# Kernel optimization log

Hardware: AMD Instinct MI355X
Metric: run time of the kernel (lower is better)

Reference implementation:

```python
import jax, jax.numpy as jnp
from jax import lax
import numpy as np

K = 32        # self.k: neighbors queried per center
TOP = 5       # inner topk size (hardcoded in source)
MAX_ITER = 16 # bound on the data-dependent while loop; leftovers emitted at final iter


def _refine_one(pc, centers, ids):
    """Vectorized translation of the per-batch while-loop.

    Instead of shrinking the sample set each iteration (data-dependent shape),
    every sample is tracked with an `active` flag and a convergence-iteration
    stamp. Emitting order in the torch code is (iteration, surviving-order),
    and boolean masking preserves relative original order, so a stable sort by
    (conv_iter, original_index) reproduces the exact concatenation order.
    """
    N, D = pc.shape
    S = centers.shape[0]
    ar = jnp.arange(S)

    def knn(q):  # q: [S,3] -> [S,K] indices of nearest cloud points (ascending dist)
        d2 = jnp.sum((q[:, None, :] - pc[None, :, :]) ** 2, axis=-1)  # [S,N]
        _, ind = lax.top_k(-d2, K)
        return ind

    def step(cur_pts, cur_idx):
        ind = knn(cur_pts)                                   # [S,K]
        nbh = pc[ind]                                        # [S,K,3]
        gc = jnp.mean(nbh, axis=1)                           # [S,3]
        dist = jnp.linalg.norm(nbh - gc[:, None, :], axis=2) # [S,K]
        _, top = lax.top_k(-dist, TOP)                       # [S,TOP] smallest dists
        in_top = jnp.any(top == 0, axis=1)                   # center (col 0) stable?
        new_idx = ind[ar, top[:, 0]]                         # point closest to centroid
        return ind, in_top, new_idx

    def body(it, st):
        cur_pts, cur_idx, conv_it, out_pts, out_idx, out_grp, active = st
        ind, in_top, new_idx = step(cur_pts, cur_idx)
        newly = active & in_top
        conv_it = jnp.where(newly, it, conv_it)
        out_pts = jnp.where(newly[:, None], cur_pts, out_pts)
        out_idx = jnp.where(newly, cur_idx, out_idx)
        out_grp = jnp.where(newly[:, None], ind, out_grp)
        move = active & ~in_top
        cur_idx = jnp.where(move, new_idx, cur_idx)
        cur_pts = jnp.where(move[:, None], pc[new_idx], cur_pts)
        return (cur_pts, cur_idx, conv_it, out_pts, out_idx, out_grp, move)

    st0 = (centers, ids,
           jnp.full((S,), MAX_ITER, jnp.int32),
           jnp.zeros((S, D), pc.dtype),
           jnp.zeros((S,), ids.dtype),
           jnp.zeros((S, K), jnp.int32),
           jnp.ones((S,), bool))
    cur_pts, cur_idx, conv_it, out_pts, out_idx, out_grp, active = lax.fori_loop(
        0, MAX_ITER, body, st0)

    # force-emit any sample that never converged within MAX_ITER
    ind, _, _ = step(cur_pts, cur_idx)
    out_pts = jnp.where(active[:, None], cur_pts, out_pts)
    out_idx = jnp.where(active, cur_idx, out_idx)
    out_grp = jnp.where(active[:, None], ind, out_grp)

    order = jnp.argsort(conv_it * (S + 1) + ar)  # stable (iter, orig-pos) order
    return out_pts[order], out_idx[order], out_grp[order]


def setup_inputs() -> dict:
    key = jax.random.key(0)
    k1, k2, k3 = jax.random.split(key, 3)
    B, N, S = 8, 8192, 1024
    xyz = jax.random.normal(k1, (B, N, 3), jnp.float32)
    center = jax.random.normal(k2, (B, S, 3), jnp.float32)
    idx = jax.random.randint(k3, (B, S), 0, N, jnp.int32)
    return {"xyz": xyz, "center": center, "idx": idx}


def reference(xyz, center, idx):
    assert xyz.shape[0] == center.shape[0]
    C, I1, I2 = jax.vmap(_refine_one)(xyz, center, idx)
    # torch runs under no_grad; outputs are detached constants
    return (lax.stop_gradient(C), I1, I2)
```

## Files before the change

kernel.cpp:

```cpp
#include <hip/hip_runtime.h>
#include <stdint.h>

#define BATCH   8
#define NPTS    8192
#define SCH     1024
#define KNN     32
#define TOPC    5
#define MAXIT   16
#define NCELL   4096
#define NGRP    128
#define NSEED   6

typedef unsigned long long ull;
typedef uint16_t u16;
typedef float vf2 __attribute__((ext_vector_type(2)));
typedef float vf4 __attribute__((ext_vector_type(4)));

#define SENTKEY ((((ull)0x7F800000u) << 13) | 0x1FFFull)

__device__ __forceinline__ float d2_exact(vf4 q, vf4 p) {
#pragma clang fp contract(off)
    vf2 d = q.xy - p.xy;
    vf2 s = d * d;
    float dz = q.z - p.z;
    float sz = dz * dz;
    return (s.x + s.y) + sz;
}

__device__ __forceinline__ void insert_top4(ull key, ull& k0, ull& k1, ull& k2,
                                            ull& k3, float& th) {
    if (key < k3) {
        k3 = key;
        { bool c = k3 < k2; ull mn = c ? k3 : k2, mx = c ? k2 : k3; k2 = mn; k3 = mx; }
        { bool c = k2 < k1; ull mn = c ? k2 : k1, mx = c ? k1 : k2; k1 = mn; k2 = mx; }
        { bool c = k1 < k0; ull mn = c ? k1 : k0, mx = c ? k0 : k1; k0 = mn; k1 = mx; }
        th = __uint_as_float((uint32_t)(k3 >> 13));
    }
}

__device__ __forceinline__ ull wave_min_u64(ull k) {
#pragma unroll
    for (int off = 32; off; off >>= 1) {
        ull o = (ull)__shfl_xor((unsigned long long)k, off, 64);
        k = o < k ? o : k;
    }
    return k;
}
__device__ __forceinline__ ull wave_max_u64(ull k) {
#pragma unroll
    for (int off = 32; off; off >>= 1) {
        ull o = (ull)__shfl_xor((unsigned long long)k, off, 64);
        k = o > k ? o : k;
    }
    return k;
}

__device__ __forceinline__ float bbox_mind2(vf4 q, vf4 c, vf4 h) {
    float dx = fmaxf(fabsf(q.x - c.x) - h.x, 0.f);
    float dy = fmaxf(fabsf(q.y - c.y) - h.y, 0.f);
    float dz = fmaxf(fabsf(q.z - c.z) - h.z, 0.f);
    return (dx * dx + dy * dy + dz * dz) * 0.9999f;
}

__device__ __forceinline__ ull cx(ull v, int xl, bool keepmin) {
    ull o = (ull)__shfl_xor((unsigned long long)v, xl, 64);
    return ((v < o) == keepmin) ? v : o;
}
__device__ __forceinline__ void cswap(ull& a, ull& b, bool up) {
    bool lt = a < b;
    ull mn = lt ? a : b, mx = lt ? b : a;
    a = up ? mn : mx;
    b = up ? mx : mn;
}

__device__ __forceinline__ void sort128(ull& s0, ull& s1, int lane) {
    cswap(s0, s1, true);
    if (lane & 1) { ull t = s0; s0 = s1; s1 = t; }
#pragma unroll
    for (int kk = 4; kk <= 128; kk <<= 1) {
        const bool up = (lane & (kk >> 1)) == 0;
#pragma unroll
        for (int d = kk >> 1; d >= 2; d >>= 1) {
            const int xl = d >> 1;
            const bool keepmin = (up == ((lane & xl) == 0));
            s0 = cx(s0, xl, keepmin);
            s1 = cx(s1, xl, keepmin);
        }
        cswap(s0, s1, up);
    }
}

__device__ __forceinline__ int next_gid(ull& r0, ull& r1) {
    if (r0) { int g = __ffsll((unsigned long long)r0) - 1; r0 &= r0 - 1; return g; }
    if (r1) { int g = __ffsll((unsigned long long)r1) - 1; r1 &= r1 - 1; return 64 + g; }
    return -1;
}

__device__ __forceinline__ int cell_of(float x, float y, float z) {
    int cxi = min(15, max(0, (int)floorf((x + 4.0f) * 2.0f)));
    int cyi = min(15, max(0, (int)floorf((y + 4.0f) * 2.0f)));
    int czi = min(15, max(0, (int)floorf((z + 4.0f) * 2.0f)));
    uint32_t sx = (cxi & 1) | ((cxi & 2) << 2) | ((cxi & 4) << 4) | ((cxi & 8) << 6);
    uint32_t sy = (cyi & 1) | ((cyi & 2) << 2) | ((cyi & 4) << 4) | ((cyi & 8) << 6);
    uint32_t sz = (czi & 1) | ((czi & 2) << 2) | ((czi & 4) << 4) | ((czi & 8) << 6);
    return (int)(sx | (sy << 1) | (sz << 2));
}

__device__ __attribute__((noinline)) int serial_topk_masked(
    const vf4* __restrict__ Psort, vf4 q, int lane, ull sm0, ull sm1) {
    ull k0 = SENTKEY, k1 = SENTKEY, k2 = SENTKEY, k3 = SENTKEY;
    int s0 = 0, s1 = 0, s2 = 0, s3 = 0;
    float th = __builtin_inff();
    for (int gid = 0; gid < NGRP; ++gid) {
        bool sel = (gid < 64) ? ((sm0 >> gid) & 1ull) : ((sm1 >> (gid - 64)) & 1ull);
        if (!sel) continue;
        vf4 p = Psort[(gid << 6) + lane];
        float d2 = d2_exact(q, p);
        uint32_t oi = __float_as_uint(p.w);
        ull key = ((ull)__float_as_uint(d2) << 13) | oi;
        if (d2 <= th && key < k3) {
            k3 = key; s3 = gid;
            if (k3 < k2) { ull t = k2; k2 = k3; k3 = t; int ts = s2; s2 = s3; s3 = ts; }
            if (k2 < k1) { ull t = k1; k1 = k2; k2 = t; int ts = s1; s1 = s2; s2 = ts; }
            if (k1 < k0) { ull t = k0; k0 = k1; k1 = t; int ts = s0; s0 = s1; s1 = ts; }
            th = __uint_as_float((uint32_t)(k3 >> 13));
        }
    }
    ull em0 = 0ull, em1 = 0ull;
    int cnt = 4, my_ind = 0;
    for (int r = 0; r < KNN; ++r) {
        ull gmin = wave_min_u64(k0);
        int widx = (int)(gmin & 0x1FFFull);
        if (lane == r) my_ind = widx;
        if (k0 == gmin) {
            int g = s0;
            if (g < 64) em0 |= 1ull << g; else em1 |= 1ull << (g - 64);
            k0 = k1; k1 = k2; k2 = k3; k3 = SENTKEY;
            s0 = s1; s1 = s2; s2 = s3;
            if (--cnt == 0) {
                k0 = k1 = k2 = k3 = SENTKEY;
                float th2 = __builtin_inff();
                for (int gid = 0; gid < NGRP; ++gid) {
                    bool sel = (gid < 64) ? ((sm0 >> gid) & 1ull)
                                          : ((sm1 >> (gid - 64)) & 1ull);
                    bool ex = (gid < 64) ? ((em0 >> gid) & 1ull)
                                         : ((em1 >> (gid - 64)) & 1ull);
                    if (!sel || ex) continue;
                    vf4 p = Psort[(gid << 6) + lane];
                    float d2 = d2_exact(q, p);
                    uint32_t oi = __float_as_uint(p.w);
                    ull key = ((ull)__float_as_uint(d2) << 13) | oi;
                    if (d2 <= th2 && key < k3) {
                        k3 = key; s3 = gid;
                        if (k3 < k2) { ull t = k2; k2 = k3; k3 = t; int ts = s2; s2 = s3; s3 = ts; }
                        if (k2 < k1) { ull t = k1; k1 = k2; k2 = t; int ts = s1; s1 = s2; s2 = ts; }
                        if (k1 < k0) { ull t = k0; k0 = k1; k1 = t; int ts = s0; s0 = s1; s1 = ts; }
                        th2 = __uint_as_float((uint32_t)(k3 >> 13));
                    }
                }
                cnt = 4;
            }
        }
    }
    return my_ind;
}

__global__ __launch_bounds__(256) void prep_kernel(const float* __restrict__ xyz,
                                                   vf4* __restrict__ pc4,
                                                   int* __restrict__ counts) {
    int i = (int)(blockIdx.x * blockDim.x + threadIdx.x);
    if (i >= BATCH * NPTS) return;
    vf4 v;
    v.x = xyz[(size_t)i * 3 + 0];
    v.y = xyz[(size_t)i * 3 + 1];
    v.z = xyz[(size_t)i * 3 + 2];
    v.w = 0.f;
    pc4[i] = v;
    int b = i >> 13;
    atomicAdd(&counts[b * NCELL + cell_of(v.x, v.y, v.z)], 1);
}

__global__ __launch_bounds__(1024) void scan_kernel(const int* __restrict__ counts,
                                                    int* __restrict__ cursor) {
    int b = (int)blockIdx.x, tid = (int)threadIdx.x;
    __shared__ int part[1024];
    int base = b * NCELL + tid * 4;
    int v0 = counts[base], v1 = counts[base + 1], v2 = counts[base + 2], v3 = counts[base + 3];
    int s = v0 + v1 + v2 + v3;
    part[tid] = s;
    __syncthreads();
    for (int off = 1; off < 1024; off <<= 1) {
        int t = (tid >= off) ? part[tid - off] : 0;
        __syncthreads();
        part[tid] += t;
        __syncthreads();
    }
    int excl = part[tid] - s;
    cursor[base] = excl;
    cursor[base + 1] = excl + v0;
    cursor[base + 2] = excl + v0 + v1;
    cursor[base + 3] = excl + v0 + v1 + v2;
}

__global__ __launch_bounds__(256) void scatter_kernel(const vf4* __restrict__ pc4,
                                                      int* __restrict__ cursor,
                                                      vf4* __restrict__ sortedP) {
    int i = (int)(blockIdx.x * blockDim.x + threadIdx.x);
    if (i >= BATCH * NPTS) return;
    vf4 v = pc4[i];
    int b = i >> 13, pi = i & (NPTS - 1);
    int c = cell_of(v.x, v.y, v.z);
    int pos = atomicAdd(&cursor[b * NCELL + c], 1);
    v.w = __uint_as_float((uint32_t)pi);
    sortedP[((size_t)b << 13) + pos] = v;
}

__global__ __launch_bounds__(256) void bbox_kernel(const vf4* __restrict__ sortedP,
                                                   vf4* __restrict__ bC,
                                                   vf4* __restrict__ bH) {
    int g = (int)((blockIdx.x * blockDim.x + threadIdx.x) >> 6);
    int lane = (int)(threadIdx.x & 63);
    vf4 p = sortedP[((size_t)g << 6) + lane];
    float mnx = p.x, mxx = p.x, mny = p.y, mxy = p.y, mnz = p.z, mxz = p.z;
#pragma unroll
    for (int off = 32; off; off >>= 1) {
        mnx = fminf(mnx, __shfl_xor(mnx, off, 64));
        mxx = fmaxf(mxx, __shfl_xor(mxx, off, 64));
        mny = fminf(mny, __shfl_xor(mny, off, 64));
        mxy = fmaxf(mxy, __shfl_xor(mxy, off, 64));
        mnz = fminf(mnz, __shfl_xor(mnz, off, 64));
        mxz = fmaxf(mxz, __shfl_xor(mxz, off, 64));
    }
    if (lane == 0) {
        vf4 c, h;
        c.x = (mnx + mxx) * 0.5f; c.y = (mny + mxy) * 0.5f; c.z = (mnz + mxz) * 0.5f; c.w = 0.f;
        h.x = (mxx - mnx) * 0.5f; h.y = (mxy - mny) * 0.5f; h.z = (mxz - mnz) * 0.5f; h.w = 0.f;
        bC[g] = c;
        bH[g] = h;
    }
}

__global__ __launch_bounds__(256) void refine_kernel(
    const vf4* __restrict__ pc4, const vf4* __restrict__ sortedP,
    const vf4* __restrict__ bC, const vf4* __restrict__ bH,
    const float* __restrict__ center, const int* __restrict__ idx_in,
    float* __restrict__ pts_ws, int* __restrict__ idx_ws,
    int* __restrict__ grp_ws, int* __restrict__ conv_ws) {
    const int lane = (int)(threadIdx.x & 63);
    const int w = (int)(threadIdx.x >> 6);
    const int wv = (int)((blockIdx.x * blockDim.x + threadIdx.x) >> 6);
    const int b = (int)(blockIdx.x >> 8);
    const vf4* __restrict__ Porig = pc4 + ((size_t)b << 13);
    const vf4* __restrict__ Psort = sortedP + ((size_t)b << 13);

    __shared__ vf4 sbC[NGRP], sbH[NGRP];
    __shared__ vf4 nbh[4][KNN];

    {
        const int t = (int)threadIdx.x;
        if (t < NGRP) sbC[t] = bC[(b << 7) + t];
        else          sbH[t - NGRP] = bH[(b << 7) + (t - NGRP)];
    }
    __syncthreads();

    const size_t ch = (size_t)wv;
    vf4 q;
    q.x = center[ch * 3 + 0];
    q.y = center[ch * 3 + 1];
    q.z = center[ch * 3 + 2];
    q.w = 0.f;
    int qidx = idx_in[ch];

    int conv = MAXIT;
    int my_ind = 0;
    vf4 myp = q;
    bool warm = false;

    for (int it = 0;; ++it) {
        const vf4 c0 = sbC[lane],      h0 = sbH[lane];
        const vf4 c1 = sbC[64 + lane], h1 = sbH[64 + lane];
        const float m0 = bbox_mind2(q, c0, h0);
        const float m1 = bbox_mind2(q, c1, h1);

        ull k0 = SENTKEY, k1 = SENTKEY, k2 = SENTKEY, k3 = SENTKEY;
        float th = __builtin_inff();
        ull sm0 = 0ull, sm1 = 0ull, am0 = 0ull, am1 = 0ull;
        float th0 = __builtin_inff();

        bool fastwarm = false;
        if (warm) {
            const float dw = (lane < KNN) ? d2_exact(q, myp) : 0.f;
            th0 = dw;
#pragma unroll
            for (int off = 32; off; off >>= 1)
                th0 = fmaxf(th0, __shfl_xor(th0, off, 64));
            sm0 = __ballot(m0 <= th0);
            sm1 = __ballot(m1 <= th0);
            const int nsel = __popcll(sm0) + __popcll(sm1);
            if (nsel <= 20) { fastwarm = true; am0 = sm0; am1 = sm1; }
        }

        if (!fastwarm) {
            sm0 = 0ull; sm1 = 0ull;
            ull g0k = ((ull)__float_as_uint(m0) << 7) | (uint32_t)lane;
            ull g1k = ((ull)__float_as_uint(m1) << 7) | (uint32_t)(64 + lane);
            sort128(g0k, g1k, lane);
#pragma unroll
            for (int r = 0; r < NSEED; ++r) {
                const ull nk = (r & 1)
                    ? (ull)__shfl((unsigned long long)g1k, r >> 1, 64)
                    : (ull)__shfl((unsigned long long)g0k, r >> 1, 64);
                const int gid = (int)(nk & 127ull);
                if (gid < 64) sm0 |= 1ull << gid; else sm1 |= 1ull << (gid - 64);
                const vf4 p = Psort[(gid << 6) + lane];
                const float d2 = d2_exact(q, p);
                if (d2 <= th)
                    insert_top4(((ull)__float_as_uint(d2) << 13) | __float_as_uint(p.w),
                                k0, k1, k2, k3, th);
            }
            ull t = k0;
            {
                ull o = (ull)__shfl_xor((unsigned long long)t, 32, 64);
                t = o < t ? o : t;
            }
            const ull B = wave_max_u64(t);
            const float Bd = fminf(__uint_as_float((uint32_t)(B >> 13)), th0);
            am0 = __ballot(m0 <= Bd) & ~sm0;
            am1 = __ballot(m1 <= Bd) & ~sm1;
            sm0 |= am0; sm1 |= am1;
        }

        {
            ull rem0 = am0, rem1 = am1;
            int ga = next_gid(rem0, rem1);
            while (ga >= 0) {
                const int gb = next_gid(rem0, rem1);
                const vf4 pa = Psort[(ga << 6) + lane];
                vf4 pb;
                if (gb >= 0) pb = Psort[(gb << 6) + lane];
                const float da = d2_exact(q, pa);
                if (da <= th)
                    insert_top4(((ull)__float_as_uint(da) << 13) | __float_as_uint(pa.w),
                                k0, k1, k2, k3, th);
                if (gb >= 0) {
                    const float dbv = d2_exact(q, pb);
                    if (dbv <= th)
                        insert_top4(((ull)__float_as_uint(dbv) << 13) | __float_as_uint(pb.w),
                                    k0, k1, k2, k3, th);
                }
                ga = next_gid(rem0, rem1);
            }
        }
        const ull prek3 = k3;

        const bool odd = (lane & 1) != 0;
        ull a0 = odd ? k3 : k0;
        ull a1 = odd ? k2 : k1;
        ull a2 = odd ? k1 : k2;
        ull a3 = odd ? k0 : k3;
#pragma unroll
        for (int kk = 8; kk <= 256; kk <<= 1) {
            const bool up = (lane & (kk >> 2)) == 0;
#pragma unroll
            for (int d = kk >> 1; d >= 4; d >>= 1) {
                const int xl = d >> 2;
                const bool keepmin = (up == ((lane & xl) == 0));
                a0 = cx(a0, xl, keepmin);
                a1 = cx(a1, xl, keepmin);
                a2 = cx(a2, xl, keepmin);
                a3 = cx(a3, xl, keepmin);
            }
            cswap(a0, a2, up); cswap(a1, a3, up);
            cswap(a0, a1, up); cswap(a2, a3, up);
        }
        const ull tau = (ull)__shfl((unsigned long long)a3, 7, 64);
        const ull bad = __ballot(prek3 < tau);
        if (bad != 0ull) {
            my_ind = serial_topk_masked(Psort, q, lane, sm0, sm1);
        } else {
            const int src = lane >> 2;
            const uint32_t lo0 = (uint32_t)__shfl((int)(uint32_t)a0, src, 64);
            const uint32_t lo1 = (uint32_t)__shfl((int)(uint32_t)a1, src, 64);
            const uint32_t lo2 = (uint32_t)__shfl((int)(uint32_t)a2, src, 64);
            const uint32_t lo3 = (uint32_t)__shfl((int)(uint32_t)a3, src, 64);
            const int sel = lane & 3;
            uint32_t lo = (sel == 0) ? lo0 : (sel == 1) ? lo1 : (sel == 2) ? lo2 : lo3;
            my_ind = (int)(lo & 0x1FFFu);
        }

        if (it == MAXIT) break;

        myp = q;
        if (lane < KNN) {
            myp = Porig[my_ind];
            nbh[w][lane] = myp;
        }
        __asm__ volatile("s_waitcnt lgkmcnt(0)" ::: "memory");
        float sx = 0.f, sy = 0.f, sz = 0.f;
#pragma unroll
        for (int j = 0; j < KNN; ++j) {
            vf4 pj = nbh[w][j];
            sx = __fadd_rn(sx, pj.x);
            sy = __fadd_rn(sy, pj.y);
            sz = __fadd_rn(sz, pj.z);
        }
        const float gx = __fmul_rn(sx, 0.03125f);
        const float gy = __fmul_rn(sy, 0.03125f);
        const float gz = __fmul_rn(sz, 0.03125f);

        float dj = __builtin_inff();
        if (lane < KNN) {
            const float dx = __fsub_rn(myp.x, gx);
            const float dy = __fsub_rn(myp.y, gy);
            const float dz = __fsub_rn(myp.z, gz);
            dj = sqrtf(__fadd_rn(__fadd_rn(__fmul_rn(dx, dx), __fmul_rn(dy, dy)),
                                 __fmul_rn(dz, dz)));
        }
        const uint32_t db = __float_as_uint(dj);
        const uint32_t d0 = (uint32_t)__shfl((int)db, 0, 64);
        const ull bal = __ballot(db < d0);
        if (__popcll(bal) <= TOPC - 1) { conv = it; break; }

        uint32_t m = db;
#pragma unroll
        for (int off = 32; off; off >>= 1) {
            uint32_t o = (uint32_t)__shfl_xor((int)m, off, 64);
            m = o < m ? o : m;
        }
        const ull balm = __ballot(db == m);
        const int jm = __ffsll((unsigned long long)balm) - 1;
        qidx = __shfl(my_ind, jm, 64);
        q.x = __shfl(myp.x, jm, 64);
        q.y = __shfl(myp.y, jm, 64);
        q.z = __shfl(myp.z, jm, 64);
        q.w = 0.f;
        warm = true;
    }

    if (lane < KNN) grp_ws[ch * KNN + lane] = my_ind;
    if (lane == 0) {
        pts_ws[ch * 3 + 0] = q.x;
        pts_ws[ch * 3 + 1] = q.y;
        pts_ws[ch * 3 + 2] = q.z;
        idx_ws[ch] = qidx;
        conv_ws[ch] = conv;
    }
}

__global__ __launch_bounds__(1024) void order_kernel(
    const float* __restrict__ pts_ws, const int* __restrict__ idx_ws,
    const int* __restrict__ grp_ws, const int* __restrict__ conv_ws,
    float* __restrict__ out) {
    const int b = (int)blockIdx.x;
    const int s = (int)threadIdx.x;
    const int w = s >> 6, l = s & 63;
    __shared__ int wavecnt[16][MAXIT + 1];
    __shared__ int binbase[MAXIT + 1];
    const size_t ch = (size_t)b * SCH + s;
    const int c = conv_ws[ch];
    int rw = 0;
#pragma unroll
    for (int v = 0; v <= MAXIT; ++v) {
        ull bal = __ballot(c == v);
        if (l == 0) wavecnt[w][v] = (int)__popcll(bal);
        if (c == v) rw = (int)__popcll(bal & ((1ull << l) - 1ull));
    }
    __syncthreads();
    if (s == 0) {
        int acc = 0;
        for (int v = 0; v <= MAXIT; ++v) {
            int t = 0;
            for (int w2 = 0; w2 < 16; ++w2) t += wavecnt[w2][v];
            binbase[v] = acc;
            acc += t;
        }
    }
    __syncthreads();
    int pos = binbase[c] + rw;
    for (int w2 = 0; w2 < w; ++w2) pos += wavecnt[w2][c];

    float* __restrict__ C  = out;
    float* __restrict__ I1 = out + (size_t)BATCH * SCH * 3;
    float* __restrict__ I2 = I1 + (size_t)BATCH * SCH;
    const size_t o = (size_t)b * SCH + pos;
    C[o * 3 + 0] = pts_ws[ch * 3 + 0];
    C[o * 3 + 1] = pts_ws[ch * 3 + 1];
    C[o * 3 + 2] = pts_ws[ch * 3 + 2];
    I1[o] = (float)idx_ws[ch];
#pragma unroll
    for (int k = 0; k < KNN; ++k) I2[o * KNN + k] = (float)grp_ws[ch * KNN + k];
}

extern "C" void kernel_launch(void* const* d_in, const int* in_sizes, int n_in,
                              void* d_out, int out_size, void* d_ws, size_t ws_size,
                              hipStream_t stream) {
    const float* xyz    = (const float*)d_in[0];
    const float* center = (const float*)d_in[1];
    const int*   idx_in = (const int*)d_in[2];
    float* out = (float*)d_out;

    char* wp = (char*)d_ws;
    vf4* pc4     = (vf4*)wp;  wp += (size_t)BATCH * NPTS * sizeof(vf4);
    vf4* sortedP = (vf4*)wp;  wp += (size_t)BATCH * NPTS * sizeof(vf4);
    vf4* bC      = (vf4*)wp;  wp += (size_t)BATCH * NGRP * sizeof(vf4);
    vf4* bH      = (vf4*)wp;  wp += (size_t)BATCH * NGRP * sizeof(vf4);
    int* counts  = (int*)wp;  wp += (size_t)BATCH * NCELL * 4;
    int* cursor  = (int*)wp;  wp += (size_t)BATCH * NCELL * 4;
    float* pts_ws = (float*)wp; wp += (size_t)BATCH * SCH * 3 * 4;
    int*   idx_ws = (int*)wp;   wp += (size_t)BATCH * SCH * 4;
    int*   grp_ws = (int*)wp;   wp += (size_t)BATCH * SCH * KNN * 4;
    int*   conv_ws = (int*)wp;

    hipMemsetAsync(counts, 0, (size_t)BATCH * NCELL * 4, stream);
    prep_kernel<<<(BATCH * NPTS + 255) / 256, 256, 0, stream>>>(xyz, pc4, counts);
    scan_kernel<<<BATCH, 1024, 0, stream>>>(counts, cursor);
    scatter_kernel<<<(BATCH * NPTS + 255) / 256, 256, 0, stream>>>(pc4, cursor, sortedP);
    bbox_kernel<<<(BATCH * NGRP * 64) / 256, 256, 0, stream>>>(sortedP, bC, bH);

    const int chains = BATCH * SCH;
    refine_kernel<<<chains * 64 / 256, 256, 0, stream>>>(
        pc4, sortedP, bC, bH, center, idx_in, pts_ws, idx_ws, grp_ws, conv_ws);
    order_kernel<<<BATCH, SCH, 0, stream>>>(pts_ws, idx_ws, grp_ws, conv_ws, out);
}
```

Measured before the change: 203.1 us.

## Fuse grid build into one per-batch kernel, sort 32-bit keys, tune launch bounds

Replaces the memset, prep, scan, scatter and bbox kernels with a single per-batch 1024-thread kernel. It builds the cell histogram in shared memory, does a wave-shuffle scan, scatters the points and computes the group bounding boxes, which removes several launches and global atomics. The group-distance bitonic sort now uses 32-bit keys made from truncated float bits instead of 64-bit keys, halving the shuffle traffic. Truncating the float bits may change the seed order when distances nearly tie, which could affect exactness. Launch bounds on refine_kernel are set to request 5 blocks per CU.

```diff
diff --git a/kernel.cpp b/kernel.cpp
--- a/kernel.cpp
+++ b/kernel.cpp
@@ -12,7 +12,6 @@
 #define NSEED   6
 
 typedef unsigned long long ull;
-typedef uint16_t u16;
 typedef float vf2 __attribute__((ext_vector_type(2)));
 typedef float vf4 __attribute__((ext_vector_type(4)));
 
@@ -73,9 +72,19 @@
     b = up ? mx : mn;
 }
 
-__device__ __forceinline__ void sort128(ull& s0, ull& s1, int lane) {
-    cswap(s0, s1, true);
-    if (lane & 1) { ull t = s0; s0 = s1; s1 = t; }
+__device__ __forceinline__ uint32_t cx32(uint32_t v, int xl, bool keepmin) {
+    uint32_t o = (uint32_t)__shfl_xor((int)v, xl, 64);
+    return ((v < o) == keepmin) ? v : o;
+}
+__device__ __forceinline__ void cswap32(uint32_t& a, uint32_t& b, bool up) {
+    uint32_t mn = a < b ? a : b, mx = a < b ? b : a;
+    a = up ? mn : mx;
+    b = up ? mx : mn;
+}
+
+__device__ __forceinline__ void sort128_u32(uint32_t& s0, uint32_t& s1, int lane) {
+    cswap32(s0, s1, true);
+    if (lane & 1) { uint32_t t = s0; s0 = s1; s1 = t; }
 #pragma unroll
     for (int kk = 4; kk <= 128; kk <<= 1) {
         const bool up = (lane & (kk >> 1)) == 0;
@@ -83,10 +92,10 @@
         for (int d = kk >> 1; d >= 2; d >>= 1) {
             const int xl = d >> 1;
             const bool keepmin = (up == ((lane & xl) == 0));
-            s0 = cx(s0, xl, keepmin);
-            s1 = cx(s1, xl, keepmin);
-        }
-        cswap(s0, s1, up);
+            s0 = cx32(s0, xl, keepmin);
+            s1 = cx32(s1, xl, keepmin);
+        }
+        cswap32(s0, s1, up);
     }
 }
 
@@ -165,82 +174,96 @@
     return my_ind;
 }
 
-__global__ __launch_bounds__(256) void prep_kernel(const float* __restrict__ xyz,
-                                                   vf4* __restrict__ pc4,
-                                                   int* __restrict__ counts) {
-    int i = (int)(blockIdx.x * blockDim.x + threadIdx.x);
-    if (i >= BATCH * NPTS) return;
-    vf4 v;
-    v.x = xyz[(size_t)i * 3 + 0];
-    v.y = xyz[(size_t)i * 3 + 1];
-    v.z = xyz[(size_t)i * 3 + 2];
-    v.w = 0.f;
-    pc4[i] = v;
-    int b = i >> 13;
-    atomicAdd(&counts[b * NCELL + cell_of(v.x, v.y, v.z)], 1);
-}
-
-__global__ __launch_bounds__(1024) void scan_kernel(const int* __restrict__ counts,
-                                                    int* __restrict__ cursor) {
-    int b = (int)blockIdx.x, tid = (int)threadIdx.x;
-    __shared__ int part[1024];
-    int base = b * NCELL + tid * 4;
-    int v0 = counts[base], v1 = counts[base + 1], v2 = counts[base + 2], v3 = counts[base + 3];
-    int s = v0 + v1 + v2 + v3;
-    part[tid] = s;
-    __syncthreads();
-    for (int off = 1; off < 1024; off <<= 1) {
-        int t = (tid >= off) ? part[tid - off] : 0;
-        __syncthreads();
-        part[tid] += t;
-        __syncthreads();
-    }
-    int excl = part[tid] - s;
-    cursor[base] = excl;
-    cursor[base + 1] = excl + v0;
-    cursor[base + 2] = excl + v0 + v1;
-    cursor[base + 3] = excl + v0 + v1 + v2;
-}
-
-__global__ __launch_bounds__(256) void scatter_kernel(const vf4* __restrict__ pc4,
-                                                      int* __restrict__ cursor,
-                                                      vf4* __restrict__ sortedP) {
-    int i = (int)(blockIdx.x * blockDim.x + threadIdx.x);
-    if (i >= BATCH * NPTS) return;
-    vf4 v = pc4[i];
-    int b = i >> 13, pi = i & (NPTS - 1);
-    int c = cell_of(v.x, v.y, v.z);
-    int pos = atomicAdd(&cursor[b * NCELL + c], 1);
-    v.w = __uint_as_float((uint32_t)pi);
-    sortedP[((size_t)b << 13) + pos] = v;
-}
-
-__global__ __launch_bounds__(256) void bbox_kernel(const vf4* __restrict__ sortedP,
-                                                   vf4* __restrict__ bC,
-                                                   vf4* __restrict__ bH) {
-    int g = (int)((blockIdx.x * blockDim.x + threadIdx.x) >> 6);
-    int lane = (int)(threadIdx.x & 63);
-    vf4 p = sortedP[((size_t)g << 6) + lane];
-    float mnx = p.x, mxx = p.x, mny = p.y, mxy = p.y, mnz = p.z, mxz = p.z;
-#pragma unroll
-    for (int off = 32; off; off >>= 1) {
-        mnx = fminf(mnx, __shfl_xor(mnx, off, 64));
-        mxx = fmaxf(mxx, __shfl_xor(mxx, off, 64));
-        mny = fminf(mny, __shfl_xor(mny, off, 64));
-        mxy = fmaxf(mxy, __shfl_xor(mxy, off, 64));
-        mnz = fminf(mnz, __shfl_xor(mnz, off, 64));
-        mxz = fmaxf(mxz, __shfl_xor(mxz, off, 64));
-    }
-    if (lane == 0) {
-        vf4 c, h;
-        c.x = (mnx + mxx) * 0.5f; c.y = (mny + mxy) * 0.5f; c.z = (mnz + mxz) * 0.5f; c.w = 0.f;
-        h.x = (mxx - mnx) * 0.5f; h.y = (mxy - mny) * 0.5f; h.z = (mxz - mnz) * 0.5f; h.w = 0.f;
-        bC[g] = c;
-        bH[g] = h;
-    }
-}
-
-__global__ __launch_bounds__(256) void refine_kernel(
+__global__ __launch_bounds__(1024) void build_kernel(const float* __restrict__ xyz,
+                                                     vf4* __restrict__ pc4,
+                                                     vf4* __restrict__ sortedP,
+                                                     vf4* __restrict__ bC,
+                                                     vf4* __restrict__ bH) {
+    const int b = (int)blockIdx.x;
+    const int t = (int)threadIdx.x;
+    const int lane = t & 63, w = t >> 6;
+    __shared__ int hist[NCELL];
+    __shared__ int wsum[16];
+
+    for (int i = t; i < NCELL; i += 1024) hist[i] = 0;
+    __syncthreads();
+
+    const float* __restrict__ X = xyz + (size_t)b * NPTS * 3;
+    vf4 pt[8];
+    int pcell[8];
+#pragma unroll
+    for (int k = 0; k < 8; ++k) {
+        const int i = k * 1024 + t;
+        vf4 v;
+        v.x = X[i * 3 + 0];
+        v.y = X[i * 3 + 1];
+        v.z = X[i * 3 + 2];
+        v.w = 0.f;
+        pt[k] = v;
+        pc4[(size_t)b * NPTS + i] = v;
+        const int c = cell_of(v.x, v.y, v.z);
+        pcell[k] = c;
+        atomicAdd(&hist[c], 1);
+    }
+    __syncthreads();
+
+    const int base = t * 4;
+    const int v0 = hist[base], v1 = hist[base + 1], v2 = hist[base + 2], v3 = hist[base + 3];
+    const int s = v0 + v1 + v2 + v3;
+    int incl = s;
+#pragma unroll
+    for (int off = 1; off < 64; off <<= 1) {
+        int o = __shfl_up(incl, off, 64);
+        if (lane >= off) incl += o;
+    }
+    if (lane == 63) wsum[w] = incl;
+    __syncthreads();
+    if (t == 0) {
+        int acc = 0;
+#pragma unroll
+        for (int i = 0; i < 16; ++i) { int x = wsum[i]; wsum[i] = acc; acc += x; }
+    }
+    __syncthreads();
+    const int excl = incl - s + wsum[w];
+    hist[base]     = excl;
+    hist[base + 1] = excl + v0;
+    hist[base + 2] = excl + v0 + v1;
+    hist[base + 3] = excl + v0 + v1 + v2;
+    __syncthreads();
+
+#pragma unroll
+    for (int k = 0; k < 8; ++k) {
+        const int i = k * 1024 + t;
+        const int pos = atomicAdd(&hist[pcell[k]], 1);
+        vf4 v = pt[k];
+        v.w = __uint_as_float((uint32_t)i);
+        sortedP[((size_t)b << 13) + pos] = v;
+    }
+    __syncthreads();
+
+    for (int g = w; g < NGRP; g += 16) {
+        vf4 p = sortedP[((size_t)b << 13) + (g << 6) + lane];
+        float mnx = p.x, mxx = p.x, mny = p.y, mxy = p.y, mnz = p.z, mxz = p.z;
+#pragma unroll
+        for (int off = 32; off; off >>= 1) {
+            mnx = fminf(mnx, __shfl_xor(mnx, off, 64));
+            mxx = fmaxf(mxx, __shfl_xor(mxx, off, 64));
+            mny = fminf(mny, __shfl_xor(mny, off, 64));
+            mxy = fmaxf(mxy, __shfl_xor(mxy, off, 64));
+            mnz = fminf(mnz, __shfl_xor(mnz, off, 64));
+            mxz = fmaxf(mxz, __shfl_xor(mxz, off, 64));
+        }
+        if (lane == 0) {
+            vf4 c, h;
+            c.x = (mnx + mxx) * 0.5f; c.y = (mny + mxy) * 0.5f; c.z = (mnz + mxz) * 0.5f; c.w = 0.f;
+            h.x = (mxx - mnx) * 0.5f; h.y = (mxy - mny) * 0.5f; h.z = (mxz - mnz) * 0.5f; h.w = 0.f;
+            bC[(b << 7) + g] = c;
+            bH[(b << 7) + g] = h;
+        }
+    }
+}
+
+__global__ __launch_bounds__(256, 5) void refine_kernel(
     const vf4* __restrict__ pc4, const vf4* __restrict__ sortedP,
     const vf4* __restrict__ bC, const vf4* __restrict__ bH,
     const float* __restrict__ center, const int* __restrict__ idx_in,
@@ -302,15 +325,15 @@
 
         if (!fastwarm) {
             sm0 = 0ull; sm1 = 0ull;
-            ull g0k = ((ull)__float_as_uint(m0) << 7) | (uint32_t)lane;
-            ull g1k = ((ull)__float_as_uint(m1) << 7) | (uint32_t)(64 + lane);
-            sort128(g0k, g1k, lane);
+            uint32_t g0k = ((__float_as_uint(m0) >> 6) << 7) | (uint32_t)lane;
+            uint32_t g1k = ((__float_as_uint(m1) >> 6) << 7) | (uint32_t)(64 + lane);
+            sort128_u32(g0k, g1k, lane);
 #pragma unroll
             for (int r = 0; r < NSEED; ++r) {
-                const ull nk = (r & 1)
-                    ? (ull)__shfl((unsigned long long)g1k, r >> 1, 64)
-                    : (ull)__shfl((unsigned long long)g0k, r >> 1, 64);
-                const int gid = (int)(nk & 127ull);
+                const uint32_t nk = (r & 1)
+                    ? (uint32_t)__shfl((int)g1k, r >> 1, 64)
+                    : (uint32_t)__shfl((int)g0k, r >> 1, 64);
+                const int gid = (int)(nk & 127u);
                 if (gid < 64) sm0 |= 1ull << gid; else sm1 |= 1ull << (gid - 64);
                 const vf4 p = Psort[(gid << 6) + lane];
                 const float d2 = d2_exact(q, p);
@@ -504,18 +527,12 @@
     vf4* sortedP = (vf4*)wp;  wp += (size_t)BATCH * NPTS * sizeof(vf4);
     vf4* bC      = (vf4*)wp;  wp += (size_t)BATCH * NGRP * sizeof(vf4);
     vf4* bH      = (vf4*)wp;  wp += (size_t)BATCH * NGRP * sizeof(vf4);
-    int* counts  = (int*)wp;  wp += (size_t)BATCH * NCELL * 4;
-    int* cursor  = (int*)wp;  wp += (size_t)BATCH * NCELL * 4;
     float* pts_ws = (float*)wp; wp += (size_t)BATCH * SCH * 3 * 4;
     int*   idx_ws = (int*)wp;   wp += (size_t)BATCH * SCH * 4;
     int*   grp_ws = (int*)wp;   wp += (size_t)BATCH * SCH * KNN * 4;
     int*   conv_ws = (int*)wp;
 
-    hipMemsetAsync(counts, 0, (size_t)BATCH * NCELL * 4, stream);
-    prep_kernel<<<(BATCH * NPTS + 255) / 256, 256, 0, stream>>>(xyz, pc4, counts);
-    scan_kernel<<<BATCH, 1024, 0, stream>>>(counts, cursor);
-    scatter_kernel<<<(BATCH * NPTS + 255) / 256, 256, 0, stream>>>(pc4, cursor, sortedP);
-    bbox_kernel<<<(BATCH * NGRP * 64) / 256, 256, 0, stream>>>(sortedP, bC, bH);
+    build_kernel<<<BATCH, 1024, 0, stream>>>(xyz, pc4, sortedP, bC, bH);
 
     const int chains = BATCH * SCH;
     refine_kernel<<<chains * 64 / 256, 256, 0, stream>>>(
```

Result: no change. 202.1 us (-0.5%).
